# Performance work log

Measured on AMD Instinct MI355X. Metric: run time of the kernel, lower is better.

The kernel has to match this reference:

```python
import jax, jax.numpy as jnp
import numpy as np

M, K, N = 32, 4096, 12288


def setup_inputs() -> dict:
    key = jax.random.key(0)
    k1, k2, k3, k4 = jax.random.split(key, 4)
    x = jax.random.normal(k1, (M, K), dtype=jnp.float32)
    # uint8-valued packed weight (stored as int32 for harness compatibility, values in [0,256))
    weight_u8 = jax.random.randint(k2, (K, N), 0, 256, dtype=jnp.int32)
    # per-output-channel fp16 scale and zero-point
    scale = (jax.random.uniform(k3, (N,), dtype=jnp.float32) * 0.01 + 1e-3).astype(jnp.float16)
    zero = (jax.random.uniform(k4, (N,), dtype=jnp.float32) * 255.0).astype(jnp.float16)
    return {"x": x, "weight_u8": weight_u8, "scale": scale, "zero": zero}


def reference(x, weight_u8, scale, zero):
    # QuantMatmulCustom: dequantize uint8 weight with per-channel fp16 scale/zero, then matmul.
    # w_deq[k, n] = (w_u8[k, n] - zero[n]) * scale[n]
    w_deq = (weight_u8.astype(jnp.float32) - zero.astype(jnp.float32)[None, :]) * scale.astype(jnp.float32)[None, :]
    # [M, K] @ [K, N] -> [M, N]
    return jnp.einsum('mk,kn->mn', x, w_deq)
```

## Files before the change

kernel.cpp:

```cpp
#include <hip/hip_runtime.h>

#define M_DIM 32
#define K_DIM 4096
#define N_DIM 12288
#define SPLITK 8
#define KPER  (K_DIM / SPLITK)
#define NT    (KPER / 32)
#define BLK   512
#define NPB   128

using bf16x8 = __attribute__((ext_vector_type(8))) short;
using f32x4  = __attribute__((ext_vector_type(4))) float;

typedef __attribute__((address_space(1))) const void GASV;
typedef __attribute__((address_space(3))) void LASV;

__device__ __forceinline__ short to_bf16(float f) {
    unsigned u = __float_as_uint(f);
    u += 0x7FFFu + ((u >> 16) & 1u);
    return (short)(u >> 16);
}

__device__ __forceinline__ bf16x8 pack_b(const int (&wv)[8]) {
    union { unsigned u[4]; bf16x8 v; } r;
    #pragma unroll
    for (int p = 0; p < 4; ++p) {
        unsigned a = __float_as_uint((float)wv[2 * p]);
        unsigned b = __float_as_uint((float)wv[2 * p + 1]);
        r.u[p] = __builtin_amdgcn_perm(b, a, 0x07060302);
    }
    return r.v;
}

__global__ __launch_bounds__(256) void qmm_prep(const float* __restrict__ x,
                                                short* __restrict__ frag,
                                                float* __restrict__ rowsum,
                                                float* __restrict__ out) {
    const int tid = threadIdx.x;
    const int bid = blockIdx.x;

    ((float4*)out)[bid * 256 + tid] = make_float4(0.f, 0.f, 0.f, 0.f);
    if (bid >= 32) return;
    const int b = bid;

    __shared__ float red[256];
    const float4* xr = (const float4*)(x + (size_t)b * K_DIM);
    float s = 0.f;
    #pragma unroll
    for (int i = 0; i < K_DIM / 4 / 256; ++i) {
        float4 v = xr[tid + 256 * i];
        s += v.x + v.y + v.z + v.w;
    }
    red[tid] = s;
    __syncthreads();
    #pragma unroll
    for (int off = 128; off > 0; off >>= 1) {
        if (tid < off) red[tid] += red[tid + off];
        __syncthreads();
    }
    if (tid == 0) rowsum[b] = red[0];

    #pragma unroll
    for (int i = 0; i < 2; ++i) {
        const int s2   = i * 256 + tid;
        const int kt   = 4 * b + (s2 >> 7);
        const int h    = (s2 >> 6) & 1;
        const int lane = s2 & 63;
        const int g    = lane >> 4;
        const int m    = 16 * h + (lane & 15);
        const float* xp = x + (size_t)m * K_DIM + kt * 32 + 8 * g;
        bf16x8 v;
        #pragma unroll
        for (int j = 0; j < 8; ++j) v[j] = to_bf16(xp[j]);
        *(bf16x8*)&frag[(size_t)((kt * 2 + h) * 64 + lane) * 8] = v;
    }
}

__global__ __launch_bounds__(BLK, 6) void qmm_main(const short* __restrict__ frag,
                                                   const int* __restrict__ w,
                                                   const float* __restrict__ rowsum,
                                                   const float* __restrict__ scale,
                                                   const float* __restrict__ zero,
                                                   float* __restrict__ out) {
    __shared__ int lds_b[2 * 32 * 128];

    const int tid  = threadIdx.x;
    const int lane = tid & 63;
    const int g    = lane >> 4;
    const int c    = lane & 15;
    const int wid  = tid >> 6;
    const int k0   = blockIdx.y * KPER;
    const int n0   = blockIdx.x * NPB;
    const int n0w  = n0 + wid * 16;

    const int* gs[2];
    #pragma unroll
    for (int q = 0; q < 2; ++q) {
        const int rl = 4 * wid + 2 * q + (lane >> 5);
        const int gg = (rl >> 3) & 3;
        const int sw = gg | ((gg & 1) << 2);
        gs[q] = w + (size_t)(k0 + rl) * N_DIM + n0 + 4 * ((lane & 31) ^ sw);
    }
    int* const ld0 = &lds_b[(wid * 2 + 0) * 256];
    int* const ld1 = &lds_b[(wid * 2 + 1) * 256];

    const int prd = (wid * 16 + c) ^ (g << 2) ^ ((g & 1) << 4);
    const int* const bq = lds_b + g * 8 * 128 + prd;

    const short* asrc = frag + ((size_t)(blockIdx.y * NT) * 1024 + lane * 8);

    f32x4 acc0 = {0.f, 0.f, 0.f, 0.f};
    f32x4 acc1 = {0.f, 0.f, 0.f, 0.f};
    bf16x8 a0, a1;

#define STAGE(T) do { if ((T) < NT) {                                            \
    __builtin_amdgcn_global_load_lds((GASV*)(gs[0] + (size_t)(32 * (T)) * N_DIM), \
        (LASV*)(ld0 + ((T) & 1) * 4096), 16, 0, 0);                              \
    __builtin_amdgcn_global_load_lds((GASV*)(gs[1] + (size_t)(32 * (T)) * N_DIM), \
        (LASV*)(ld1 + ((T) & 1) * 4096), 16, 0, 0);                              \
} } while (0)

#define LOADA(T) do {                                                            \
    a0 = *(const bf16x8*)(asrc + (size_t)(T) * 1024);                            \
    a1 = *(const bf16x8*)(asrc + (size_t)(T) * 1024 + 512);                      \
} while (0)

#define COMP(T) do {                                                             \
    const int* bp = bq + ((T) & 1) * 4096;                                       \
    int wv[8];                                                                   \
    _Pragma("unroll")                                                            \
    for (int j = 0; j < 8; ++j) wv[j] = bp[j * 128];                             \
    bf16x8 bfv = pack_b(wv);                                                     \
    acc0 = __builtin_amdgcn_mfma_f32_16x16x32_bf16(a0, bfv, acc0, 0, 0, 0);      \
    acc1 = __builtin_amdgcn_mfma_f32_16x16x32_bf16(a1, bfv, acc1, 0, 0, 0);      \
} while (0)

#define ITER(T) do { LOADA(T); COMP(T); __syncthreads(); STAGE((T) + 2); } while (0)

    STAGE(0); STAGE(1);
    __syncthreads();

    ITER(0);  ITER(1);  ITER(2);  ITER(3);
    ITER(4);  ITER(5);  ITER(6);  ITER(7);
    ITER(8);  ITER(9);  ITER(10); ITER(11);
    ITER(12); ITER(13); ITER(14);
    LOADA(15); COMP(15);

#undef STAGE
#undef LOADA
#undef COMP
#undef ITER

    const float sc = scale[n0w + c];
    float corr0[4] = {0.f, 0.f, 0.f, 0.f}, corr1[4] = {0.f, 0.f, 0.f, 0.f};
    if (blockIdx.y == 0) {
        const float zp = zero[n0w + c];
        #pragma unroll
        for (int i = 0; i < 4; ++i) {
            const int r = 4 * (lane >> 4) + i;
            corr0[i] = zp * rowsum[r];
            corr1[i] = zp * rowsum[16 + r];
        }
    }
    #pragma unroll
    for (int i = 0; i < 4; ++i) {
        const int r = 4 * (lane >> 4) + i;
        atomicAdd(&out[(size_t)r * N_DIM + n0w + c],        sc * (acc0[i] - corr0[i]));
        atomicAdd(&out[(size_t)(16 + r) * N_DIM + n0w + c], sc * (acc1[i] - corr1[i]));
    }
}

__global__ __launch_bounds__(256) void qmm_zero_fb(float* __restrict__ out) {
    int i = blockIdx.x * 256 + threadIdx.x;
    ((float4*)out)[i] = make_float4(0.f, 0.f, 0.f, 0.f);
}
__global__ __launch_bounds__(256) void qmm_main_fb(const float* __restrict__ x,
                                                   const int* __restrict__ w,
                                                   float* __restrict__ out) {
    const int n  = blockIdx.x * 256 + threadIdx.x;
    const int k0 = blockIdx.y * 256;
    float acc[M_DIM];
    #pragma unroll
    for (int m = 0; m < M_DIM; ++m) acc[m] = 0.f;
    const int* wp = w + (size_t)k0 * N_DIM + n;
    for (int kk = 0; kk < 256; kk += 4) {
        const float w0 = (float)wp[(size_t)(kk + 0) * N_DIM];
        const float w1 = (float)wp[(size_t)(kk + 1) * N_DIM];
        const float w2 = (float)wp[(size_t)(kk + 2) * N_DIM];
        const float w3 = (float)wp[(size_t)(kk + 3) * N_DIM];
        #pragma unroll
        for (int m = 0; m < M_DIM; ++m) {
            const float4 xv = *(const float4*)(x + (size_t)m * K_DIM + k0 + kk);
            acc[m] = fmaf(xv.x, w0, fmaf(xv.y, w1, fmaf(xv.z, w2, fmaf(xv.w, w3, acc[m]))));
        }
    }
    #pragma unroll
    for (int m = 0; m < M_DIM; ++m)
        atomicAdd(&out[(size_t)m * N_DIM + n], acc[m]);
}
__global__ __launch_bounds__(256) void qmm_scale_fb(const float* __restrict__ x,
                                                    const float* __restrict__ scale,
                                                    const float* __restrict__ zero,
                                                    float* __restrict__ out) {
    const int m = blockIdx.y;
    __shared__ float red[256];
    float s = 0.f;
    for (int k = threadIdx.x; k < K_DIM; k += 256)
        s += x[(size_t)m * K_DIM + k];
    red[threadIdx.x] = s;
    __syncthreads();
    #pragma unroll
    for (int off = 128; off > 0; off >>= 1) {
        if (threadIdx.x < off) red[threadIdx.x] += red[threadIdx.x + off];
        __syncthreads();
    }
    const float rowsum = red[0];
    const int n = blockIdx.x * 256 + threadIdx.x;
    const float v = out[(size_t)m * N_DIM + n];
    out[(size_t)m * N_DIM + n] = scale[n] * (v - zero[n] * rowsum);
}

extern "C" void kernel_launch(void* const* d_in, const int* in_sizes, int n_in,
                              void* d_out, int out_size, void* d_ws, size_t ws_size,
                              hipStream_t stream) {
    const float* x     = (const float*)d_in[0];
    const int*   w     = (const int*)d_in[1];
    const float* scale = (const float*)d_in[2];
    const float* zero  = (const float*)d_in[3];
    float* out = (float*)d_out;

    const size_t frag_sz = (size_t)128 * 2 * 64 * 8 * sizeof(short);
    short* fragp  = (short*)d_ws;
    float* rowsum = (float*)((char*)d_ws + frag_sz);

    if (ws_size >= frag_sz + 256) {
        qmm_prep<<<dim3(M_DIM * N_DIM / 4 / 256), dim3(256), 0, stream>>>(x, fragp, rowsum, out);
        qmm_main<<<dim3(N_DIM / NPB, SPLITK),     dim3(BLK), 0, stream>>>(fragp, w, rowsum, scale, zero, out);
    } else {
        qmm_zero_fb <<<dim3(M_DIM * N_DIM / 4 / 256), dim3(256), 0, stream>>>(out);
        qmm_main_fb <<<dim3(N_DIM / 256, 16),         dim3(256), 0, stream>>>(x, w, out);
        qmm_scale_fb<<<dim3(N_DIM / 256, M_DIM),      dim3(256), 0, stream>>>(x, scale, zero, out);
    }
}
```

Baseline: 43.59 us.

## Triple-buffer LDS weight tiles with explicit vmcnt waits and scheduling fences

Moves the weight tile staging from double to triple buffering in LDS, so tiles are prefetched three steps ahead. Explicit `s_waitcnt vmcnt` counts, `s_barrier` and `sched_barrier` fences replace `__syncthreads` to control how global-to-LDS loads overlap with the MFMA work. The activation-fragment loads are reissued inside each body step, and the source keeps some dead prologue loads and unused macros. The larger LDS footprint lowers the number of resident blocks per CU, and each iteration now has two barriers.

```diff
diff --git a/kernel.cpp b/kernel.cpp
--- a/kernel.cpp
+++ b/kernel.cpp
@@ -82,7 +82,7 @@
                                                    const float* __restrict__ scale,
                                                    const float* __restrict__ zero,
                                                    float* __restrict__ out) {
-    __shared__ int lds_b[2 * 32 * 128];
+    __shared__ int lds_b[3 * 32 * 128];
 
     const int tid  = threadIdx.x;
     const int lane = tid & 63;
@@ -113,20 +113,27 @@
     f32x4 acc1 = {0.f, 0.f, 0.f, 0.f};
     bf16x8 a0, a1;
 
+#define FENCE() __builtin_amdgcn_sched_barrier(0)
+
 #define STAGE(T) do { if ((T) < NT) {                                            \
     __builtin_amdgcn_global_load_lds((GASV*)(gs[0] + (size_t)(32 * (T)) * N_DIM), \
-        (LASV*)(ld0 + ((T) & 1) * 4096), 16, 0, 0);                              \
+        (LASV*)(ld0 + ((T) % 3) * 4096), 16, 0, 0);                              \
     __builtin_amdgcn_global_load_lds((GASV*)(gs[1] + (size_t)(32 * (T)) * N_DIM), \
-        (LASV*)(ld1 + ((T) & 1) * 4096), 16, 0, 0);                              \
-} } while (0)
-
-#define LOADA(T) do {                                                            \
+        (LASV*)(ld1 + ((T) % 3) * 4096), 16, 0, 0);                              \
+} FENCE(); } while (0)
+
+#define LOADA(T) do { if ((T) < NT) {                                            \
     a0 = *(const bf16x8*)(asrc + (size_t)(T) * 1024);                            \
     a1 = *(const bf16x8*)(asrc + (size_t)(T) * 1024 + 512);                      \
-} while (0)
+} FENCE(); } while (0)
+
+#define WAITV(N) do { asm volatile("s_waitcnt vmcnt(" #N ")" ::: "memory");      \
+    FENCE(); } while (0)
+
+#define BAR() do { FENCE(); __builtin_amdgcn_s_barrier(); FENCE(); } while (0)
 
 #define COMP(T) do {                                                             \
-    const int* bp = bq + ((T) & 1) * 4096;                                       \
+    const int* bp = bq + ((T) % 3) * 4096;                                       \
     int wv[8];                                                                   \
     _Pragma("unroll")                                                            \
     for (int j = 0; j < 8; ++j) wv[j] = bp[j * 128];                             \
@@ -135,21 +142,63 @@
     acc1 = __builtin_amdgcn_mfma_f32_16x16x32_bf16(a1, bfv, acc1, 0, 0, 0);      \
 } while (0)
 
-#define ITER(T) do { LOADA(T); COMP(T); __syncthreads(); STAGE((T) + 2); } while (0)
-
-    STAGE(0); STAGE(1);
-    __syncthreads();
-
-    ITER(0);  ITER(1);  ITER(2);  ITER(3);
-    ITER(4);  ITER(5);  ITER(6);  ITER(7);
-    ITER(8);  ITER(9);  ITER(10); ITER(11);
-    ITER(12); ITER(13); ITER(14);
-    LOADA(15); COMP(15);
-
+#define ITER(T, NW) do {                                                         \
+    WAITV(NW); BAR();                                                            \
+    bf16x8 na0 = a0, na1 = a1; (void)na0; (void)na1;                             \
+    COMP(T);                                                                     \
+    BAR();                                                                       \
+    STAGE((T) + 3); LOADA((T) + 2);                                              \
+} while (0)
+
+    STAGE(0); STAGE(1); LOADA(0); STAGE(2);
+    WAITV(4); BAR();
+    bf16x8 c0 = a0, c1 = a1;
+    LOADA(1);
+    {
+        const int* bp = bq;
+        int wv[8];
+        #pragma unroll
+        for (int j = 0; j < 8; ++j) wv[j] = bp[j * 128];
+        bf16x8 bfv = pack_b(wv);
+        acc0 = __builtin_amdgcn_mfma_f32_16x16x32_bf16(c0, bfv, acc0, 0, 0, 0);
+        acc1 = __builtin_amdgcn_mfma_f32_16x16x32_bf16(c1, bfv, acc1, 0, 0, 0);
+    }
+    BAR();
+    STAGE(3); LOADA(2);
+#define ITER2(T, NW) do {                                                        \
+    WAITV(NW); BAR();                                                            \
+    bf16x8 s0 = a0, s1 = a1;    \
+     \
+     \
+    (void)s0; (void)s1;                                                          \
+    COMP(T);                                                                     \
+    BAR();                                                                       \
+    STAGE((T) + 3); LOADA((T) + 2);                                              \
+} while (0)
+
+#undef ITER
+#undef ITER2
+
+#define BODY(T, NW) do {                                                         \
+    LOADA(T);                                     \
+    WAITV(NW); BAR();                          \
+    COMP(T);                                                                     \
+    BAR();                                                                       \
+    STAGE((T) + 3);                                                              \
+} while (0)
+
+    BODY(1, 4);  BODY(2, 4);  BODY(3, 4);  BODY(4, 4);
+    BODY(5, 4);  BODY(6, 4);  BODY(7, 4);  BODY(8, 4);
+    BODY(9, 4);  BODY(10, 4); BODY(11, 4); BODY(12, 4);
+    BODY(13, 2); BODY(14, 2); BODY(15, 0);
+
+#undef BODY
 #undef STAGE
 #undef LOADA
+#undef WAITV
+#undef BAR
 #undef COMP
-#undef ITER
+#undef FENCE
 
     const float sc = scale[n0w + c];
     float corr0[4] = {0.f, 0.f, 0.f, 0.f}, corr1[4] = {0.f, 0.f, 0.f, 0.f};
```

Measured after the change: 44.11 us. No clear change (+1.2%).
